# Kernel tuning notes

Measured on AMD Instinct MI355X. Metric: run time of the kernel, lower is better.

## Reference

```python
import jax, jax.numpy as jnp
import numpy as np

B, L, NIN, NHID, NLAYERS = 16, 2048, 1024, 1024, 2


def _gru_step_zero_h(x, W_ih, b_ih, W_hh, b_hh):
    """torch GRU cell with h_prev = 0 (faithful to the module's bug where
    hidden is never updated and starts at zeros).
    r = sigmoid(W_ir x + b_ir + b_hr)
    z = sigmoid(W_iz x + b_iz + b_hz)
    n = tanh(W_in x + b_in + r * b_hn)   # W_hn @ 0 == 0
    h = (1 - z) * n                       # + z * 0
    W_hh is unused because h_prev == 0 (kept as an arg for parity).
    """
    del W_hh
    g = jnp.einsum('blf,hf->blh', x, W_ih) + b_ih  # (B, L, 3H)
    H = b_ih.shape[0] // 3
    gi_r, gi_z, gi_n = g[..., :H], g[..., H:2 * H], g[..., 2 * H:]
    bh_r, bh_z, bh_n = b_hh[:H], b_hh[H:2 * H], b_hh[2 * H:]
    r = jax.nn.sigmoid(gi_r + bh_r)
    z = jax.nn.sigmoid(gi_z + bh_z)
    n = jnp.tanh(gi_n + r * bh_n)
    return (1.0 - z) * n


def setup_inputs() -> dict:
    key = jax.random.key(0)
    ks = jax.random.split(key, 12)
    s_in = 1.0 / np.sqrt(NIN)
    s_h = 1.0 / np.sqrt(NHID)
    inp = {
        'inputs': jax.random.normal(ks[0], (B, L, NIN), dtype=jnp.float32),
        'inputs_mask': jax.random.randint(ks[1], (B, L), 0, 2, dtype=jnp.int32),
        # layer 0 (input size NIN)
        'W_ih0': jax.random.uniform(ks[2], (3 * NHID, NIN), jnp.float32, -s_in, s_in),
        'W_hh0': jax.random.uniform(ks[3], (3 * NHID, NHID), jnp.float32, -s_h, s_h),
        'b_ih0': jax.random.uniform(ks[4], (3 * NHID,), jnp.float32, -s_h, s_h),
        'b_hh0': jax.random.uniform(ks[5], (3 * NHID,), jnp.float32, -s_h, s_h),
        # layer 1 (input size NHID)
        'W_ih1': jax.random.uniform(ks[6], (3 * NHID, NHID), jnp.float32, -s_h, s_h),
        'W_hh1': jax.random.uniform(ks[7], (3 * NHID, NHID), jnp.float32, -s_h, s_h),
        'b_ih1': jax.random.uniform(ks[8], (3 * NHID,), jnp.float32, -s_h, s_h),
        'b_hh1': jax.random.uniform(ks[9], (3 * NHID,), jnp.float32, -s_h, s_h),
    }
    return inp


def reference(inputs, inputs_mask, W_ih0, W_hh0, b_ih0, b_hh0,
              W_ih1, W_hh1, b_ih1, b_hh1):
    # hidden is never updated in the original step(), so every timestep runs
    # the 2-layer GRU one step from zero hidden -> fully parallel over time.
    h1 = _gru_step_zero_h(inputs, W_ih0, b_ih0, W_hh0, b_hh0)   # (B, L, H)
    h2 = _gru_step_zero_h(h1, W_ih1, b_ih1, W_hh1, b_hh1)       # (B, L, H)
    mask = inputs_mask.astype(h2.dtype)[..., None]               # (B, L, 1)
    # output_p * mask + hidden[0] * (1 - mask), with hidden[0] == 0
    out = h2 * mask
    # original returns (steps, b_s, nhid)
    return jnp.transpose(out, (1, 0, 2))
```

## Files before the change

### kernel.cpp

```cpp
#include <hip/hip_runtime.h>
#include <hip/hip_bf16.h>
#include <cstdint>
#include <cstddef>

#define BB 16
#define LL 2048
#define MM (BB * LL)
#define KK 1024
#define HH 1024

typedef __attribute__((ext_vector_type(8))) short bf16x8;
typedef __attribute__((ext_vector_type(4))) float f32x4;

__device__ __forceinline__ unsigned short f2bf(float f) {
    unsigned u = __builtin_bit_cast(unsigned, f);
    u += 0x7fffu + ((u >> 16) & 1u);
    return (unsigned short)(u >> 16);
}

__global__ void cvt_f32_to_bf16(const float* __restrict__ in,
                                unsigned short* __restrict__ out, int n8) {
    int i = blockIdx.x * blockDim.x + threadIdx.x;
    if (i >= n8) return;
    const float4* p = reinterpret_cast<const float4*>(in) + (size_t)i * 2;
    float4 v0 = p[0];
    float4 v1 = p[1];
    union { unsigned short us[8]; uint4 v; } o;
    o.us[0] = f2bf(v0.x); o.us[1] = f2bf(v0.y);
    o.us[2] = f2bf(v0.z); o.us[3] = f2bf(v0.w);
    o.us[4] = f2bf(v1.x); o.us[5] = f2bf(v1.y);
    o.us[6] = f2bf(v1.z); o.us[7] = f2bf(v1.w);
    reinterpret_cast<uint4*>(out)[i] = o.v;
}

__global__ __launch_bounds__(1024) void scan_mask(const int* __restrict__ mask,
                                                  int* __restrict__ rows,
                                                  int* __restrict__ Na) {
    __shared__ int psum[1024];
    const int t = threadIdx.x;
    const int base = t * 32;
    int m[32];
    int cnt = 0;
#pragma unroll
    for (int i = 0; i < 32; ++i) { m[i] = mask[base + i]; cnt += (m[i] != 0); }
    psum[t] = cnt;
    __syncthreads();
    for (int off = 1; off < 1024; off <<= 1) {
        int v = (t >= off) ? psum[t - off] : 0;
        __syncthreads();
        psum[t] += v;
        __syncthreads();
    }
    int offset = psum[t] - cnt;
#pragma unroll
    for (int i = 0; i < 32; ++i) {
        if (m[i]) rows[offset++] = base + i;
    }
    if (t == 1023) *Na = psum[1023];
}

__global__ __launch_bounds__(256) void gather_cvt(const float* __restrict__ x,
                                                  const int* __restrict__ rows,
                                                  const int* __restrict__ Na,
                                                  unsigned short* __restrict__ xbf) {
    const int j = blockIdx.x;
    if (j >= *Na) return;
    const int r = rows[j];
    const float4 v = reinterpret_cast<const float4*>(x + (size_t)r * KK)[threadIdx.x];
    ushort4 o;
    o.x = f2bf(v.x); o.y = f2bf(v.y); o.z = f2bf(v.z); o.w = f2bf(v.w);
    reinterpret_cast<ushort4*>(xbf + (size_t)j * KK)[threadIdx.x] = o;
}

__global__ __launch_bounds__(256) void zero_masked(const int* __restrict__ mask,
                                                   float* __restrict__ out) {
    const int m = blockIdx.x;
    if (mask[m] != 0) return;
    const int bb = m >> 11;
    const int ll = m & 2047;
    float4 z = {0.f, 0.f, 0.f, 0.f};
    reinterpret_cast<float4*>(out + ((size_t)ll * BB + bb) * HH)[threadIdx.x] = z;
}

__device__ __forceinline__ void gload16(const unsigned short* g, unsigned short* l) {
    __builtin_amdgcn_global_load_lds(
        (const __attribute__((address_space(1))) unsigned int*)g,
        (__attribute__((address_space(3))) unsigned int*)l,
        16, 0, 0);
}

template <int MODE>
__global__ __launch_bounds__(256, 2) void gru_layer(
    const unsigned short* __restrict__ A,
    const unsigned short* __restrict__ W,
    const float* __restrict__ b_ih,
    const float* __restrict__ b_hh,
    const int* __restrict__ rows,
    const int* __restrict__ Na_p,
    unsigned short* __restrict__ out_bf,
    float* __restrict__ out_f) {
    constexpr int BM = 128, BN = 64, BK = 32;
    __shared__ unsigned short As[BM * BK];
    __shared__ unsigned short Bs[3 * BN * BK];

    const int Na = *Na_p;
    const int m0 = blockIdx.x * BM;
    if (m0 >= Na) return;

    const int tid  = threadIdx.x;
    const int lane = tid & 63;
    const int wid  = tid >> 6;
    const int wr   = wid >> 1;
    const int wc   = wid & 1;
    const int n0 = blockIdx.y * BN;

    int ar0 = m0 + (tid >> 2);        if (ar0 >= Na) ar0 = Na - 1;
    int ar1 = m0 + 64 + (tid >> 2);   if (ar1 >= Na) ar1 = Na - 1;
    const unsigned short* a_src0 = A + (size_t)ar0 * KK + (tid & 3) * 8;
    const unsigned short* a_src1 = A + (size_t)ar1 * KK + (tid & 3) * 8;
    const unsigned short* b_src0 = W + (size_t)(0 * HH + n0 + (tid >> 2)) * KK + (tid & 3) * 8;
    const unsigned short* b_src1 = W + (size_t)(1 * HH + n0 + (tid >> 2)) * KK + (tid & 3) * 8;
    const unsigned short* b_src2 = W + (size_t)(2 * HH + n0 + (tid >> 2)) * KK + (tid & 3) * 8;
    unsigned short* a_dst0 = &As[wid * 512];
    unsigned short* a_dst1 = &As[2048 + wid * 512];
    unsigned short* b_dst0 = &Bs[0 * 2048 + wid * 512];
    unsigned short* b_dst1 = &Bs[1 * 2048 + wid * 512];
    unsigned short* b_dst2 = &Bs[2 * 2048 + wid * 512];

    int a_off[4], b_off[2];
#pragma unroll
    for (int mf = 0; mf < 4; ++mf)
        a_off[mf] = (wr * 64 + mf * 16 + (lane & 15)) * BK + (lane >> 4) * 8;
#pragma unroll
    for (int nf = 0; nf < 2; ++nf)
        b_off[nf] = (wc * 32 + nf * 16 + (lane & 15)) * BK + (lane >> 4) * 8;

    f32x4 accr[4][2] = {};
    f32x4 accz[4][2] = {};
    f32x4 accn[4][2] = {};

    for (int k0 = 0; k0 < KK; k0 += BK) {
        __syncthreads();
        gload16(a_src0 + k0, a_dst0);
        gload16(a_src1 + k0, a_dst1);
        gload16(b_src0 + k0, b_dst0);
        gload16(b_src1 + k0, b_dst1);
        gload16(b_src2 + k0, b_dst2);
        __syncthreads();

        bf16x8 af[4];
#pragma unroll
        for (int mf = 0; mf < 4; ++mf)
            af[mf] = *reinterpret_cast<const bf16x8*>(&As[a_off[mf]]);
#pragma unroll
        for (int nf = 0; nf < 2; ++nf) {
            bf16x8 br  = *reinterpret_cast<const bf16x8*>(&Bs[b_off[nf]]);
            bf16x8 bz  = *reinterpret_cast<const bf16x8*>(&Bs[2048 + b_off[nf]]);
            bf16x8 bnn = *reinterpret_cast<const bf16x8*>(&Bs[4096 + b_off[nf]]);
#pragma unroll
            for (int mf = 0; mf < 4; ++mf) {
                accr[mf][nf] = __builtin_amdgcn_mfma_f32_16x16x32_bf16(af[mf], br,  accr[mf][nf], 0, 0, 0);
                accz[mf][nf] = __builtin_amdgcn_mfma_f32_16x16x32_bf16(af[mf], bz,  accz[mf][nf], 0, 0, 0);
                accn[mf][nf] = __builtin_amdgcn_mfma_f32_16x16x32_bf16(af[mf], bnn, accn[mf][nf], 0, 0, 0);
            }
        }
    }

#pragma unroll
    for (int nf = 0; nf < 2; ++nf) {
        const int col = n0 + wc * 32 + nf * 16 + (lane & 15);
        const float br_b = b_ih[col] + b_hh[col];
        const float bz_b = b_ih[HH + col] + b_hh[HH + col];
        const float bn_i = b_ih[2 * HH + col];
        const float bn_h = b_hh[2 * HH + col];
#pragma unroll
        for (int mf = 0; mf < 4; ++mf) {
#pragma unroll
            for (int j = 0; j < 4; ++j) {
                const int row = m0 + wr * 64 + mf * 16 + (lane >> 4) * 4 + j;
                if (row >= Na) continue;
                const float r = 1.f / (1.f + __expf(-(accr[mf][nf][j] + br_b)));
                const float z = 1.f / (1.f + __expf(-(accz[mf][nf][j] + bz_b)));
                const float n = tanhf(accn[mf][nf][j] + bn_i + r * bn_h);
                const float h = (1.f - z) * n;
                if (MODE == 0) {
                    out_bf[(size_t)row * HH + col] = f2bf(h);
                } else {
                    const int orig = rows[row];
                    const int bb = orig >> 11;
                    const int ll = orig & 2047;
                    out_f[((size_t)ll * BB + bb) * HH + col] = h;
                }
            }
        }
    }
}

extern "C" void kernel_launch(void* const* d_in, const int* in_sizes, int n_in,
                              void* d_out, int out_size, void* d_ws, size_t ws_size,
                              hipStream_t stream) {
    const float* x   = (const float*)d_in[0];
    const int*   msk = (const int*)d_in[1];
    const float* W0  = (const float*)d_in[2];
    const float* bi0 = (const float*)d_in[4];
    const float* bh0 = (const float*)d_in[5];
    const float* W1  = (const float*)d_in[6];
    const float* bi1 = (const float*)d_in[8];
    const float* bh1 = (const float*)d_in[9];
    float* out = (float*)d_out;

    char* ws = (char*)d_ws;
    unsigned short* xbf  = (unsigned short*)ws;
    unsigned short* h1bf = (unsigned short*)(ws + 67108864);
    unsigned short* w0bf = (unsigned short*)(ws + 134217728);
    unsigned short* w1bf = (unsigned short*)(ws + 140509184);
    int* rows = (int*)(ws + 146800640);
    int* Na   = (int*)(ws + 146931712);

    scan_mask<<<1, 1024, 0, stream>>>(msk, rows, Na);

    cvt_f32_to_bf16<<<1536, 256, 0, stream>>>(W0, w0bf, 3 * HH * KK / 8);
    cvt_f32_to_bf16<<<1536, 256, 0, stream>>>(W1, w1bf, 3 * HH * KK / 8);

    zero_masked<<<MM, 256, 0, stream>>>(msk, out);

    gather_cvt<<<MM, 256, 0, stream>>>(x, rows, Na, xbf);

    dim3 grid(MM / 128, HH / 64);
    gru_layer<0><<<grid, 256, 0, stream>>>(xbf, w0bf, bi0, bh0, rows, Na, h1bf, nullptr);
    gru_layer<1><<<grid, 256, 0, stream>>>(h1bf, w1bf, bi1, bh1, rows, Na, nullptr, out);
}
```

Baseline: 374.5 us.

## Double-buffer LDS with async prefetch and larger 256x64 tiles in GRU GEMM

Rewrites the fused GRU GEMM kernel to use 512-thread blocks with 256x64 output tiles and BK=64. Global-to-LDS loads for the next K tile are issued into a second LDS buffer while MFMAs run on the current one, using explicit vmcnt waits, sched barriers and setprio. The LDS layout is XOR-swizzled to avoid bank conflicts. The aim is to hide global-load latency and raise MFMA utilization. In exchange it uses more LDS (about 112KB per block) and more accumulator registers, which may lower occupancy.

```diff
diff --git a/kernel.cpp b/kernel.cpp
--- a/kernel.cpp
+++ b/kernel.cpp
@@ -89,8 +89,15 @@
         16, 0, 0);
 }
 
+#define WAITVM2 asm volatile("s_waitcnt vmcnt(2)" ::: "memory")
+#define WAITVM7 asm volatile("s_waitcnt vmcnt(7)" ::: "memory")
+#define WAITVM0 asm volatile("s_waitcnt vmcnt(0)" ::: "memory")
+#define WAITLG0 asm volatile("s_waitcnt lgkmcnt(0)" ::: "memory")
+#define SB      __builtin_amdgcn_sched_barrier(0)
+#define BAR     __builtin_amdgcn_s_barrier()
+
 template <int MODE>
-__global__ __launch_bounds__(256, 2) void gru_layer(
+__global__ __launch_bounds__(512, 2) void gru_layer(
     const unsigned short* __restrict__ A,
     const unsigned short* __restrict__ W,
     const float* __restrict__ b_ih,
@@ -99,101 +106,163 @@
     const int* __restrict__ Na_p,
     unsigned short* __restrict__ out_bf,
     float* __restrict__ out_f) {
-    constexpr int BM = 128, BN = 64, BK = 32;
-    __shared__ unsigned short As[BM * BK];
-    __shared__ unsigned short Bs[3 * BN * BK];
+    __shared__ unsigned short lds[2][28672];
 
     const int Na = *Na_p;
-    const int m0 = blockIdx.x * BM;
+    const int m0 = blockIdx.x * 256;
     if (m0 >= Na) return;
+    const int n0 = blockIdx.y * 64;
 
     const int tid  = threadIdx.x;
     const int lane = tid & 63;
     const int wid  = tid >> 6;
-    const int wr   = wid >> 1;
-    const int wc   = wid & 1;
-    const int n0 = blockIdx.y * BN;
-
-    int ar0 = m0 + (tid >> 2);        if (ar0 >= Na) ar0 = Na - 1;
-    int ar1 = m0 + 64 + (tid >> 2);   if (ar1 >= Na) ar1 = Na - 1;
-    const unsigned short* a_src0 = A + (size_t)ar0 * KK + (tid & 3) * 8;
-    const unsigned short* a_src1 = A + (size_t)ar1 * KK + (tid & 3) * 8;
-    const unsigned short* b_src0 = W + (size_t)(0 * HH + n0 + (tid >> 2)) * KK + (tid & 3) * 8;
-    const unsigned short* b_src1 = W + (size_t)(1 * HH + n0 + (tid >> 2)) * KK + (tid & 3) * 8;
-    const unsigned short* b_src2 = W + (size_t)(2 * HH + n0 + (tid >> 2)) * KK + (tid & 3) * 8;
-    unsigned short* a_dst0 = &As[wid * 512];
-    unsigned short* a_dst1 = &As[2048 + wid * 512];
-    unsigned short* b_dst0 = &Bs[0 * 2048 + wid * 512];
-    unsigned short* b_dst1 = &Bs[1 * 2048 + wid * 512];
-    unsigned short* b_dst2 = &Bs[2 * 2048 + wid * 512];
-
-    int a_off[4], b_off[2];
+    const int wr   = wid >> 2;
+    const int wc   = wid & 3;
+
+    const int trow = tid >> 3;
+    const int tcol = ((tid & 7) ^ (trow & 7)) * 8;
+    int r0 = m0 + trow;        if (r0 >= Na) r0 = Na - 1;
+    int r1 = m0 + 64 + trow;   if (r1 >= Na) r1 = Na - 1;
+    int r2 = m0 + 128 + trow;  if (r2 >= Na) r2 = Na - 1;
+    int r3 = m0 + 192 + trow;  if (r3 >= Na) r3 = Na - 1;
+    const unsigned short* a0 = A + (size_t)r0 * KK + tcol;
+    const unsigned short* a1 = A + (size_t)r1 * KK + tcol;
+    const unsigned short* a2 = A + (size_t)r2 * KK + tcol;
+    const unsigned short* a3 = A + (size_t)r3 * KK + tcol;
+    const unsigned short* b0 = W + (size_t)(0 * HH + n0 + trow) * KK + tcol;
+    const unsigned short* b1 = W + (size_t)(1 * HH + n0 + trow) * KK + tcol;
+    const unsigned short* b2 = W + (size_t)(2 * HH + n0 + trow) * KK + tcol;
+
+#define STAGE(kt, c) do {                                       \
+        const int _o = (kt) * 64;                               \
+        unsigned short* _L = &lds[(c)][wid * 512];              \
+        gload16(a0 + _o, _L + 0 * 4096);                        \
+        gload16(a2 + _o, _L + 2 * 4096);                        \
+        gload16(b0 + _o, _L + 16384 + 0 * 4096);                \
+        gload16(b1 + _o, _L + 16384 + 1 * 4096);                \
+        gload16(b2 + _o, _L + 16384 + 2 * 4096);                \
+        gload16(a1 + _o, _L + 1 * 4096);                        \
+        gload16(a3 + _o, _L + 3 * 4096);                        \
+    } while (0)
+
+    const int l15  = lane & 15;
+    const int akp0 = (((lane >> 4) << 3)) ^ ((lane & 7) << 3);
+    const int akp1 = (32 + ((lane >> 4) << 3)) ^ ((lane & 7) << 3);
+    int aoff0[4], aoff1[4], boff[3];
 #pragma unroll
-    for (int mf = 0; mf < 4; ++mf)
-        a_off[mf] = (wr * 64 + mf * 16 + (lane & 15)) * BK + (lane >> 4) * 8;
+    for (int mf = 0; mf < 4; ++mf) {
+        aoff0[mf] = (wr * 128 + 0 * 64 + mf * 16 + l15) * 64;
+        aoff1[mf] = (wr * 128 + 1 * 64 + mf * 16 + l15) * 64;
+    }
 #pragma unroll
-    for (int nf = 0; nf < 2; ++nf)
-        b_off[nf] = (wc * 32 + nf * 16 + (lane & 15)) * BK + (lane >> 4) * 8;
-
-    f32x4 accr[4][2] = {};
-    f32x4 accz[4][2] = {};
-    f32x4 accn[4][2] = {};
-
-    for (int k0 = 0; k0 < KK; k0 += BK) {
-        __syncthreads();
-        gload16(a_src0 + k0, a_dst0);
-        gload16(a_src1 + k0, a_dst1);
-        gload16(b_src0 + k0, b_dst0);
-        gload16(b_src1 + k0, b_dst1);
-        gload16(b_src2 + k0, b_dst2);
-        __syncthreads();
-
-        bf16x8 af[4];
-#pragma unroll
-        for (int mf = 0; mf < 4; ++mf)
-            af[mf] = *reinterpret_cast<const bf16x8*>(&As[a_off[mf]]);
-#pragma unroll
-        for (int nf = 0; nf < 2; ++nf) {
-            bf16x8 br  = *reinterpret_cast<const bf16x8*>(&Bs[b_off[nf]]);
-            bf16x8 bz  = *reinterpret_cast<const bf16x8*>(&Bs[2048 + b_off[nf]]);
-            bf16x8 bnn = *reinterpret_cast<const bf16x8*>(&Bs[4096 + b_off[nf]]);
-#pragma unroll
-            for (int mf = 0; mf < 4; ++mf) {
-                accr[mf][nf] = __builtin_amdgcn_mfma_f32_16x16x32_bf16(af[mf], br,  accr[mf][nf], 0, 0, 0);
-                accz[mf][nf] = __builtin_amdgcn_mfma_f32_16x16x32_bf16(af[mf], bz,  accz[mf][nf], 0, 0, 0);
-                accn[mf][nf] = __builtin_amdgcn_mfma_f32_16x16x32_bf16(af[mf], bnn, accn[mf][nf], 0, 0, 0);
-            }
-        }
-    }
-
-#pragma unroll
-    for (int nf = 0; nf < 2; ++nf) {
-        const int col = n0 + wc * 32 + nf * 16 + (lane & 15);
-        const float br_b = b_ih[col] + b_hh[col];
-        const float bz_b = b_ih[HH + col] + b_hh[HH + col];
-        const float bn_i = b_ih[2 * HH + col];
-        const float bn_h = b_hh[2 * HH + col];
-#pragma unroll
-        for (int mf = 0; mf < 4; ++mf) {
-#pragma unroll
-            for (int j = 0; j < 4; ++j) {
-                const int row = m0 + wr * 64 + mf * 16 + (lane >> 4) * 4 + j;
-                if (row >= Na) continue;
-                const float r = 1.f / (1.f + __expf(-(accr[mf][nf][j] + br_b)));
-                const float z = 1.f / (1.f + __expf(-(accz[mf][nf][j] + bz_b)));
-                const float n = tanhf(accn[mf][nf][j] + bn_i + r * bn_h);
-                const float h = (1.f - z) * n;
-                if (MODE == 0) {
-                    out_bf[(size_t)row * HH + col] = f2bf(h);
-                } else {
-                    const int orig = rows[row];
-                    const int bb = orig >> 11;
-                    const int ll = orig & 2047;
-                    out_f[((size_t)ll * BB + bb) * HH + col] = h;
-                }
-            }
-        }
-    }
+    for (int g = 0; g < 3; ++g)
+        boff[g] = 16384 + g * 4096 + (wc * 16 + l15) * 64;
+
+    f32x4 acc0[4][3] = {};
+    f32x4 acc1[4][3] = {};
+    bf16x8 afrag[4];
+    bf16x8 bfrag[3];
+
+#define READ_B(Lp, akp) do {                                                   \
+        _Pragma("unroll") for (int g = 0; g < 3; ++g)                          \
+            bfrag[g] = *reinterpret_cast<const bf16x8*>(&(Lp)[boff[g] + (akp)]); \
+    } while (0)
+#define READ_A0(Lp, akp) do {                                                   \
+        _Pragma("unroll") for (int mf = 0; mf < 4; ++mf)                        \
+            afrag[mf] = *reinterpret_cast<const bf16x8*>(&(Lp)[aoff0[mf] + (akp)]); \
+    } while (0)
+#define READ_A1(Lp, akp) do {                                                   \
+        _Pragma("unroll") for (int mf = 0; mf < 4; ++mf)                        \
+            afrag[mf] = *reinterpret_cast<const bf16x8*>(&(Lp)[aoff1[mf] + (akp)]); \
+    } while (0)
+#define PHASE_MFMA(accN) do {                                                   \
+        __builtin_amdgcn_s_setprio(1);                                          \
+        _Pragma("unroll") for (int g = 0; g < 3; ++g)                           \
+            _Pragma("unroll") for (int mf = 0; mf < 4; ++mf)                    \
+                accN[mf][g] = __builtin_amdgcn_mfma_f32_16x16x32_bf16(          \
+                    afrag[mf], bfrag[g], accN[mf][g], 0, 0, 0);                 \
+        __builtin_amdgcn_s_setprio(0);                                          \
+    } while (0)
+
+    STAGE(0, 0);
+
+    int cur = 0;
+#pragma unroll 1
+    for (int kt = 0; kt < 15; ++kt) {
+        unsigned short* L = &lds[cur][0];
+        WAITVM2; BAR; SB;
+        READ_B(L, akp0); READ_A0(L, akp0);
+        STAGE(kt + 1, cur ^ 1);
+        SB;
+        WAITLG0; SB;
+        PHASE_MFMA(acc0);
+        WAITVM7; BAR; SB;
+        READ_A1(L, akp0);
+        WAITLG0; SB;
+        PHASE_MFMA(acc1);
+        READ_B(L, akp1); READ_A0(L, akp1);
+        WAITLG0; SB;
+        PHASE_MFMA(acc0);
+        READ_A1(L, akp1);
+        WAITLG0; SB;
+        PHASE_MFMA(acc1);
+        cur ^= 1;
+    }
+    {
+        unsigned short* L = &lds[cur][0];
+        WAITVM2; BAR; SB;
+        READ_B(L, akp0); READ_A0(L, akp0);
+        WAITLG0; SB;
+        PHASE_MFMA(acc0);
+        WAITVM0; BAR; SB;
+        READ_A1(L, akp0);
+        WAITLG0; SB;
+        PHASE_MFMA(acc1);
+        READ_B(L, akp1); READ_A0(L, akp1);
+        WAITLG0; SB;
+        PHASE_MFMA(acc0);
+        READ_A1(L, akp1);
+        WAITLG0; SB;
+        PHASE_MFMA(acc1);
+    }
+
+    const int col = n0 + wc * 16 + l15;
+    const float br_b = b_ih[col] + b_hh[col];
+    const float bz_b = b_ih[HH + col] + b_hh[HH + col];
+    const float bn_i = b_ih[2 * HH + col];
+    const float bn_h = b_hh[2 * HH + col];
+
+#define EPILOGUE(accN, mh) do {                                                  \
+        _Pragma("unroll") for (int mf = 0; mf < 4; ++mf) {                       \
+            _Pragma("unroll") for (int j = 0; j < 4; ++j) {                      \
+                const int row = m0 + wr * 128 + (mh) * 64 + mf * 16 +            \
+                                (lane >> 4) * 4 + j;                             \
+                if (row < Na) {                                                  \
+                    const float r = 1.f / (1.f + __expf(-(accN[mf][0][j] + br_b))); \
+                    const float z = 1.f / (1.f + __expf(-(accN[mf][1][j] + bz_b))); \
+                    const float n = tanhf(accN[mf][2][j] + bn_i + r * bn_h);     \
+                    const float h = (1.f - z) * n;                               \
+                    if (MODE == 0) {                                             \
+                        out_bf[(size_t)row * HH + col] = f2bf(h);                \
+                    } else {                                                     \
+                        const int orig = rows[row];                              \
+                        const int bb = orig >> 11;                               \
+                        const int ll = orig & 2047;                              \
+                        out_f[((size_t)ll * BB + bb) * HH + col] = h;            \
+                    }                                                            \
+                }                                                                \
+            }                                                                    \
+        }                                                                        \
+    } while (0)
+
+    EPILOGUE(acc0, 0);
+    EPILOGUE(acc1, 1);
+#undef STAGE
+#undef READ_B
+#undef READ_A0
+#undef READ_A1
+#undef PHASE_MFMA
+#undef EPILOGUE
 }
 
 extern "C" void kernel_launch(void* const* d_in, const int* in_sizes, int n_in,
@@ -223,10 +292,9 @@
     cvt_f32_to_bf16<<<1536, 256, 0, stream>>>(W1, w1bf, 3 * HH * KK / 8);
 
     zero_masked<<<MM, 256, 0, stream>>>(msk, out);
-
     gather_cvt<<<MM, 256, 0, stream>>>(x, rows, Na, xbf);
 
-    dim3 grid(MM / 128, HH / 64);
-    gru_layer<0><<<grid, 256, 0, stream>>>(xbf, w0bf, bi0, bh0, rows, Na, h1bf, nullptr);
-    gru_layer<1><<<grid, 256, 0, stream>>>(h1bf, w1bf, bi1, bh1, rows, Na, nullptr, out);
-}
+    dim3 grid(MM / 256, HH / 64);
+    gru_layer<0><<<grid, 512, 0, stream>>>(xbf, w0bf, bi0, bh0, rows, Na, h1bf, nullptr);
+    gru_layer<1><<<grid, 512, 0, stream>>>(h1bf, w1bf, bi1, bh1, rows, Na, nullptr, out);
+}
```

Result: slower. 416.6 us (+11.2%).

## Double-buffer LDS tiles with XOR swizzle and MFMA priority in GRU GEMM

Applied to the files above, without the earlier changes.

The GRU GEMM main loop now uses two LDS buffers: it issues the global-to-LDS loads for the next K-tile before computing on the current one, so each iteration needs one barrier instead of two syncthreads. The K-chunk index of each row in LDS is XOR-swizzled with the row index to reduce bank conflicts on the 16-byte fragment reads. s_setprio is raised around the MFMA bursts. LDS use doubles to 40KB per block, which may limit occupancy at two blocks per CU, and the explicit vmcnt(0) wait still serialises on load completion at the end of each step.

```diff
diff --git a/kernel.cpp b/kernel.cpp
--- a/kernel.cpp
+++ b/kernel.cpp
@@ -89,6 +89,10 @@
         16, 0, 0);
 }
 
+#define WAITVM0 asm volatile("s_waitcnt vmcnt(0)" ::: "memory")
+#define SB      __builtin_amdgcn_sched_barrier(0)
+#define BAR     __builtin_amdgcn_s_barrier()
+
 template <int MODE>
 __global__ __launch_bounds__(256, 2) void gru_layer(
     const unsigned short* __restrict__ A,
@@ -99,76 +103,94 @@
     const int* __restrict__ Na_p,
     unsigned short* __restrict__ out_bf,
     float* __restrict__ out_f) {
-    constexpr int BM = 128, BN = 64, BK = 32;
-    __shared__ unsigned short As[BM * BK];
-    __shared__ unsigned short Bs[3 * BN * BK];
+    __shared__ unsigned short lds[2][10240];
 
     const int Na = *Na_p;
-    const int m0 = blockIdx.x * BM;
+    const int m0 = blockIdx.x * 128;
     if (m0 >= Na) return;
+    const int n0 = blockIdx.y * 64;
 
     const int tid  = threadIdx.x;
     const int lane = tid & 63;
     const int wid  = tid >> 6;
     const int wr   = wid >> 1;
     const int wc   = wid & 1;
-    const int n0 = blockIdx.y * BN;
-
-    int ar0 = m0 + (tid >> 2);        if (ar0 >= Na) ar0 = Na - 1;
-    int ar1 = m0 + 64 + (tid >> 2);   if (ar1 >= Na) ar1 = Na - 1;
-    const unsigned short* a_src0 = A + (size_t)ar0 * KK + (tid & 3) * 8;
-    const unsigned short* a_src1 = A + (size_t)ar1 * KK + (tid & 3) * 8;
-    const unsigned short* b_src0 = W + (size_t)(0 * HH + n0 + (tid >> 2)) * KK + (tid & 3) * 8;
-    const unsigned short* b_src1 = W + (size_t)(1 * HH + n0 + (tid >> 2)) * KK + (tid & 3) * 8;
-    const unsigned short* b_src2 = W + (size_t)(2 * HH + n0 + (tid >> 2)) * KK + (tid & 3) * 8;
-    unsigned short* a_dst0 = &As[wid * 512];
-    unsigned short* a_dst1 = &As[2048 + wid * 512];
-    unsigned short* b_dst0 = &Bs[0 * 2048 + wid * 512];
-    unsigned short* b_dst1 = &Bs[1 * 2048 + wid * 512];
-    unsigned short* b_dst2 = &Bs[2 * 2048 + wid * 512];
-
-    int a_off[4], b_off[2];
+
+    const int trow = tid >> 2;
+    const int tcol = ((tid & 3) ^ (trow & 3)) * 8;
+    int r0 = m0 + trow;        if (r0 >= Na) r0 = Na - 1;
+    int r1 = m0 + 64 + trow;   if (r1 >= Na) r1 = Na - 1;
+    const unsigned short* a0 = A + (size_t)r0 * KK + tcol;
+    const unsigned short* a1 = A + (size_t)r1 * KK + tcol;
+    const unsigned short* b0 = W + (size_t)(0 * HH + n0 + trow) * KK + tcol;
+    const unsigned short* b1 = W + (size_t)(1 * HH + n0 + trow) * KK + tcol;
+    const unsigned short* b2 = W + (size_t)(2 * HH + n0 + trow) * KK + tcol;
+
+#define STAGE(kt, c) do {                                        \
+        const int _o = (kt) * 32;                                \
+        unsigned short* _L = &lds[(c)][wid * 512];               \
+        gload16(a0 + _o, _L + 0 * 2048);                         \
+        gload16(a1 + _o, _L + 1 * 2048);                         \
+        gload16(b0 + _o, _L + 2 * 2048);                         \
+        gload16(b1 + _o, _L + 3 * 2048);                         \
+        gload16(b2 + _o, _L + 4 * 2048);                         \
+    } while (0)
+
+    const int l15 = lane & 15;
+    const int akp = (((lane >> 4) ^ (lane & 3)) & 3) << 3;
+    int aoff[4], boff[2];
 #pragma unroll
     for (int mf = 0; mf < 4; ++mf)
-        a_off[mf] = (wr * 64 + mf * 16 + (lane & 15)) * BK + (lane >> 4) * 8;
+        aoff[mf] = (wr * 64 + mf * 16 + l15) * 32 + akp;
 #pragma unroll
     for (int nf = 0; nf < 2; ++nf)
-        b_off[nf] = (wc * 32 + nf * 16 + (lane & 15)) * BK + (lane >> 4) * 8;
+        boff[nf] = 4096 + (wc * 32 + nf * 16 + l15) * 32 + akp;
 
     f32x4 accr[4][2] = {};
     f32x4 accz[4][2] = {};
     f32x4 accn[4][2] = {};
 
-    for (int k0 = 0; k0 < KK; k0 += BK) {
-        __syncthreads();
-        gload16(a_src0 + k0, a_dst0);
-        gload16(a_src1 + k0, a_dst1);
-        gload16(b_src0 + k0, b_dst0);
-        gload16(b_src1 + k0, b_dst1);
-        gload16(b_src2 + k0, b_dst2);
-        __syncthreads();
-
-        bf16x8 af[4];
-#pragma unroll
-        for (int mf = 0; mf < 4; ++mf)
-            af[mf] = *reinterpret_cast<const bf16x8*>(&As[a_off[mf]]);
-#pragma unroll
-        for (int nf = 0; nf < 2; ++nf) {
-            bf16x8 br  = *reinterpret_cast<const bf16x8*>(&Bs[b_off[nf]]);
-            bf16x8 bz  = *reinterpret_cast<const bf16x8*>(&Bs[2048 + b_off[nf]]);
-            bf16x8 bnn = *reinterpret_cast<const bf16x8*>(&Bs[4096 + b_off[nf]]);
-#pragma unroll
-            for (int mf = 0; mf < 4; ++mf) {
-                accr[mf][nf] = __builtin_amdgcn_mfma_f32_16x16x32_bf16(af[mf], br,  accr[mf][nf], 0, 0, 0);
-                accz[mf][nf] = __builtin_amdgcn_mfma_f32_16x16x32_bf16(af[mf], bz,  accz[mf][nf], 0, 0, 0);
-                accn[mf][nf] = __builtin_amdgcn_mfma_f32_16x16x32_bf16(af[mf], bnn, accn[mf][nf], 0, 0, 0);
-            }
-        }
+#define COMPUTE(Lp) do {                                                          \
+        bf16x8 af[4];                                                             \
+        _Pragma("unroll") for (int mf = 0; mf < 4; ++mf)                          \
+            af[mf] = *reinterpret_cast<const bf16x8*>(&(Lp)[aoff[mf]]);           \
+        _Pragma("unroll") for (int nf = 0; nf < 2; ++nf) {                        \
+            bf16x8 br  = *reinterpret_cast<const bf16x8*>(&(Lp)[boff[nf]]);       \
+            bf16x8 bz  = *reinterpret_cast<const bf16x8*>(&(Lp)[boff[nf] + 2048]);\
+            bf16x8 bnn = *reinterpret_cast<const bf16x8*>(&(Lp)[boff[nf] + 4096]);\
+            __builtin_amdgcn_s_setprio(1);                                        \
+            _Pragma("unroll") for (int mf = 0; mf < 4; ++mf) {                    \
+                accr[mf][nf] = __builtin_amdgcn_mfma_f32_16x16x32_bf16(           \
+                    af[mf], br,  accr[mf][nf], 0, 0, 0);                          \
+                accz[mf][nf] = __builtin_amdgcn_mfma_f32_16x16x32_bf16(           \
+                    af[mf], bz,  accz[mf][nf], 0, 0, 0);                          \
+                accn[mf][nf] = __builtin_amdgcn_mfma_f32_16x16x32_bf16(           \
+                    af[mf], bnn, accn[mf][nf], 0, 0, 0);                          \
+            }                                                                     \
+            __builtin_amdgcn_s_setprio(0);                                        \
+        }                                                                         \
+    } while (0)
+
+    STAGE(0, 0);
+    WAITVM0; BAR; SB;
+
+    int cur = 0;
+#pragma unroll 1
+    for (int kt = 0; kt < 31; ++kt) {
+        STAGE(kt + 1, cur ^ 1);
+        const unsigned short* L = &lds[cur][0];
+        COMPUTE(L);
+        WAITVM0; BAR; SB;
+        cur ^= 1;
+    }
+    {
+        const unsigned short* L = &lds[cur][0];
+        COMPUTE(L);
     }
 
 #pragma unroll
     for (int nf = 0; nf < 2; ++nf) {
-        const int col = n0 + wc * 32 + nf * 16 + (lane & 15);
+        const int col = n0 + wc * 32 + nf * 16 + l15;
         const float br_b = b_ih[col] + b_hh[col];
         const float bz_b = b_ih[HH + col] + b_hh[HH + col];
         const float bn_i = b_ih[2 * HH + col];
@@ -194,6 +216,8 @@
             }
         }
     }
+#undef STAGE
+#undef COMPUTE
 }
 
 extern "C" void kernel_launch(void* const* d_in, const int* in_sizes, int n_in,
@@ -223,7 +247,6 @@
     cvt_f32_to_bf16<<<1536, 256, 0, stream>>>(W1, w1bf, 3 * HH * KK / 8);
 
     zero_masked<<<MM, 256, 0, stream>>>(msk, out);
-
     gather_cvt<<<MM, 256, 0, stream>>>(x, rows, Na, xbf);
 
     dim3 grid(MM / 128, HH / 64);
```

After: 350.3 us. 6.5% less time.
